# Kernel tuning notes

Hardware: AMD Instinct MI355X
Metric: run time of the kernel (lower is better)

The kernel has to match this reference:

```python
import jax, jax.numpy as jnp
import numpy as np

N = 100000       # n_nodes
E = 128          # hidden_channels
R = 9            # n_relations
L = 3            # n_layers
NE = 640000      # n_edges


def setup_inputs() -> dict:
    key = jax.random.key(0)
    k = jax.random.split(key, 5)
    edge_index = jax.random.randint(k[0], (2, NE), 0, N, dtype=jnp.int64)
    edge_type = jax.random.randint(k[1], (NE,), 0, R, dtype=jnp.int64)
    embeddings = jax.random.normal(k[2], (N, E), dtype=jnp.float32)
    # per-layer weights [L, 2R, E, E] (first R = forward direction, last R = reverse)
    weights = jax.random.normal(k[3], (L, 2 * R, E, E), dtype=jnp.float32)
    biases = jax.random.normal(k[4], (L, 2 * R, E), dtype=jnp.float32)
    return {
        "edge_index": edge_index,
        "edge_type": edge_type,
        "embeddings": embeddings,
        "weights": weights,
        "biases": biases,
    }


def reference(edge_index, edge_type, embeddings, weights, biases):
    src, dst = edge_index[0], edge_index[1]
    n_nodes = embeddings.shape[0]
    n_layers, r2 = weights.shape[0], weights.shape[1]
    n_rel = r2 // 2

    hidden = embeddings
    for l in range(n_layers):
        # NB: source code resets hidden to the embeddings at the top of each
        # layer, so each layer transforms the raw embeddings. We reproduce
        # that exactly (the relu in the source is dead code: its result is
        # immediately overwritten by `hidden = output`).
        hidden = embeddings
        # Transform node features once per relation (node-level GEMM) instead
        # of per-edge: mathematically identical to gathering then matmul.
        ht = jnp.einsum('ne,reh->rnh', hidden, weights[l])  # [2R, N, E]
        # forward direction: message = W_r @ h[src] + b_r, scattered to dst
        msg_f = ht[edge_type, src] + biases[l][edge_type]          # [NE, E]
        out = jax.ops.segment_sum(msg_f, dst, num_segments=n_nodes)
        # reverse direction: message = W_{r+R} @ h[dst] + b_{r+R}, scattered to src
        msg_b = ht[edge_type + n_rel, dst] + biases[l][edge_type + n_rel]
        out = out + jax.ops.segment_sum(msg_b, src, num_segments=n_nodes)
        hidden = out
    return hidden
```

## Files before the change

### kernel.cpp

```cpp
#include <hip/hip_runtime.h>
#include <hip/hip_bf16.h>


#define E_DIM 128
#define R_REL 9
#define TN 16
#define MT_P 1156
#define SCB 1024
#define NSLICE 96

typedef __attribute__((ext_vector_type(8))) short short8v;
typedef __attribute__((ext_vector_type(4))) float f32x4;

static __device__ __forceinline__ unsigned short f2bf(float f) {
    union { float f; unsigned u; } v; v.f = f;
    unsigned u = v.u;
    return (unsigned short)((u + 0x7FFFu + ((u >> 16) & 1u)) >> 16);
}
static __device__ __forceinline__ float bf2f(unsigned short h) {
    union { unsigned u; float f; } v; v.u = ((unsigned)h) << 16;
    return v.f;
}


__global__ __launch_bounds__(256) void prep(
    const float* __restrict__ H, const float* __restrict__ W18,
    unsigned short* __restrict__ Hbf, unsigned short* __restrict__ Wt,
    long total8)
{
    const int tid = threadIdx.x;
    if (blockIdx.x < 18) {
        const int rel = blockIdx.x;
        const float* __restrict__ Wr = W18 + (size_t)rel * E_DIM * E_DIM;
#pragma unroll
        for (int k = 0; k < 8; k++) {
            int f = tid + k * 256;
            int lane = f & 63;
            int c = (f >> 6) & 1;
            int s = (f >> 7) & 3;
            int w = (f >> 9) & 3;
            int col = w * 32 + c * 16 + (lane & 15);
            int kb = s * 32 + (lane >> 4) * 8;
            short8v v;
#pragma unroll
            for (int j = 0; j < 8; j++)
                v[j] = (short)f2bf(Wr[(size_t)(kb + j) * E_DIM + col]);
            *(short8v*)(Wt + ((size_t)((((rel * 4 + w) * 4 + s) * 2 + c) * 64 + lane)) * 8) = v;
        }
    } else {
        long i = (long)(blockIdx.x - 18) * 256 + tid;
        if (i >= total8) return;
        const float4* src = (const float4*)(H + i * 8);
        float4 a = src[0], b = src[1];
        short8v o;
        o[0] = (short)f2bf(a.x); o[1] = (short)f2bf(a.y);
        o[2] = (short)f2bf(a.z); o[3] = (short)f2bf(a.w);
        o[4] = (short)f2bf(b.x); o[5] = (short)f2bf(b.y);
        o[6] = (short)f2bf(b.z); o[7] = (short)f2bf(b.w);
        *(short8v*)(Hbf + i * 8) = o;
    }
}

__global__ __launch_bounds__(256) void k_count8(
    const int* __restrict__ esrc, const int* __restrict__ edst,
    const int* __restrict__ etype, int* __restrict__ cnt, int ne, int Nn)
{
    const int oct = blockIdx.x & 7;
    const int slice = blockIdx.x >> 3;
    const int lo = (int)(((long long)oct * Nn) >> 3);
    const int hi = (int)(((long long)(oct + 1) * Nn) >> 3);
    for (int e = slice * 256 + threadIdx.x; e < ne; e += NSLICE * 256) {
        int t = etype[e], s = esrc[e], d = edst[e];
        if (d >= lo && d < hi) atomicAdd(&cnt[d * R_REL + t], 1);
        if (s >= lo && s < hi) atomicAdd(&cnt[(Nn + s) * R_REL + t], 1);
    }
}

__global__ __launch_bounds__(256) void k_scan_part(
    const int* __restrict__ cnt, int* __restrict__ loc,
    int* __restrict__ bsum, int n2)
{
    __shared__ int sh[256];
    const int tid = threadIdx.x;
    const int i0 = blockIdx.x * SCB + tid * 4;
    int v0 = 0, v1 = 0, v2 = 0, v3 = 0;
    if (i0 + 3 < n2) {
        int4 v = *(const int4*)(cnt + i0);
        v0 = v.x; v1 = v.y; v2 = v.z; v3 = v.w;
    } else {
        if (i0 + 0 < n2) v0 = cnt[i0 + 0];
        if (i0 + 1 < n2) v1 = cnt[i0 + 1];
        if (i0 + 2 < n2) v2 = cnt[i0 + 2];
        if (i0 + 3 < n2) v3 = cnt[i0 + 3];
    }
    int t = v0 + v1 + v2 + v3;
    sh[tid] = t;
    __syncthreads();
    for (int o = 1; o < 256; o <<= 1) {
        int x = (tid >= o) ? sh[tid - o] : 0;
        __syncthreads();
        sh[tid] += x;
        __syncthreads();
    }
    int excl = sh[tid] - t;
    if (tid == 255) bsum[blockIdx.x] = sh[255];
    int p0 = excl, p1 = p0 + v0, p2 = p1 + v1, p3 = p2 + v2;
    if (i0 + 3 < n2) {
        *(int4*)(loc + i0) = make_int4(p0, p1, p2, p3);
    } else {
        if (i0 + 0 < n2) loc[i0 + 0] = p0;
        if (i0 + 1 < n2) loc[i0 + 1] = p1;
        if (i0 + 2 < n2) loc[i0 + 2] = p2;
        if (i0 + 3 < n2) loc[i0 + 3] = p3;
    }
}

__global__ __launch_bounds__(256) void k_scan_mid(int* __restrict__ bsum, int nb)
{
    __shared__ int sh[256];
    __shared__ int carry;
    const int tid = threadIdx.x;
    if (tid == 0) carry = 0;
    __syncthreads();
    for (int base = 0; base < nb; base += 256) {
        int i = base + tid;
        int v = (i < nb) ? bsum[i] : 0;
        sh[tid] = v;
        __syncthreads();
        for (int o = 1; o < 256; o <<= 1) {
            int x = (tid >= o) ? sh[tid - o] : 0;
            __syncthreads();
            sh[tid] += x;
            __syncthreads();
        }
        int excl = sh[tid] - v + carry;
        int total = sh[255];
        if (i < nb) bsum[i] = excl;
        __syncthreads();
        if (tid == 0) carry += total;
        __syncthreads();
    }
}

__global__ __launch_bounds__(256) void k_scan_apply(
    const int* __restrict__ loc, const int* __restrict__ bsum,
    int* __restrict__ off, int* __restrict__ cursor, int n2)
{
    const int add = bsum[blockIdx.x];
    const int i0 = blockIdx.x * SCB + threadIdx.x * 4;
    if (i0 + 3 < n2) {
        int4 v = *(const int4*)(loc + i0);
        v.x += add; v.y += add; v.z += add; v.w += add;
        *(int4*)(off + i0) = v;
        *(int4*)(cursor + i0) = v;
    } else {
#pragma unroll
        for (int j = 0; j < 4; j++)
            if (i0 + j < n2) {
                int v = loc[i0 + j] + add;
                off[i0 + j] = v;
                cursor[i0 + j] = v;
            }
    }
}

__global__ __launch_bounds__(256) void k_fill8(
    const int* __restrict__ esrc, const int* __restrict__ edst,
    const int* __restrict__ etype, int* __restrict__ cursor,
    unsigned* __restrict__ rec, int ne, int Nn)
{
    const int oct = blockIdx.x & 7;
    const int slice = blockIdx.x >> 3;
    const int lo = (int)(((long long)oct * Nn) >> 3);
    const int hi = (int)(((long long)(oct + 1) * Nn) >> 3);
    for (int e = slice * 256 + threadIdx.x; e < ne; e += NSLICE * 256) {
        int t = etype[e], s = esrc[e], d = edst[e];
        if (d >= lo && d < hi) {
            int p = atomicAdd(&cursor[d * R_REL + t], 1);
            rec[p] = ((unsigned)t << 20) | (unsigned)s;
        }
        if (s >= lo && s < hi) {
            int p2 = atomicAdd(&cursor[(Nn + s) * R_REL + t], 1);
            rec[p2] = ((unsigned)t << 20) | (unsigned)d;
        }
    }
}

__global__ __launch_bounds__(256, 4) void fused_rgcn(
    const unsigned short* __restrict__ Hbf, const unsigned short* __restrict__ Wt,
    const float* __restrict__ B18,
    const int* __restrict__ off3, const int* __restrict__ cur3,
    const unsigned* __restrict__ rec,
    float* __restrict__ out, int Nn)
{
    __shared__ __align__(16) unsigned short Mt[TN][MT_P];
    __shared__ float degS[2][TN][R_REL];

    const int tid = threadIdx.x;
    const int lane = tid & 63;
    const int w = tid >> 6;
    const int lr = lane & 15;
    const int lg = lane >> 4;
    const int n0 = blockIdx.x * TN;

    const short8v* wt8 = (const short8v*)Wt;

    f32x4 acc[2];
    acc[0] = (f32x4){0.f, 0.f, 0.f, 0.f};
    acc[1] = (f32x4){0.f, 0.f, 0.f, 0.f};

#define RMW(rk, vk, idx)                                                      \
    {                                                                         \
        int _t = (rk) >> 20;                                                  \
        int _nd = ((idx) >= s1) + ((idx) >= s2) + ((idx) >= s3);              \
        unsigned* _mp = (unsigned*)(&Mt[w * 4 + _nd][_t * E_DIM]) + lane;     \
        unsigned _u = *_mp;                                                   \
        float _mx = bf2f((unsigned short)(_u & 0xFFFF)) + bf2f((vk).x);       \
        float _my = bf2f((unsigned short)(_u >> 16)) + bf2f((vk).y);          \
        *_mp = ((unsigned)f2bf(_my) << 16) | (unsigned)f2bf(_mx);             \
    }

#pragma unroll 1
    for (int dir = 0; dir < 2; dir++) {
        const short8v z8 = (short8v){0, 0, 0, 0, 0, 0, 0, 0};
#pragma unroll
        for (int rr = 0; rr < 4; rr++) {
            int row = w * 4 + rr;
            *(short8v*)(&Mt[row][(size_t)lane * 8]) = z8;
            *(short8v*)(&Mt[row][(size_t)(lane + 64) * 8]) = z8;
            if (lane < 16) *(short8v*)(&Mt[row][(size_t)(lane + 128) * 8]) = z8;
        }

        const int jj = lg, tt = lr;
        const int gnode_j = n0 + w * 4 + jj;
        int blo = 0x7F000000, bhi = 0x7F000000;
        if (gnode_j < Nn && tt < R_REL) {
            size_t sb = ((size_t)(dir ? (Nn + gnode_j) : gnode_j)) * R_REL + tt;
            blo = off3[sb];
            bhi = cur3[sb];
            degS[dir][w * 4 + jj][tt] = (float)(bhi - blo);
        }

        const int nvalid = min(4, max(0, Nn - (n0 + w * 4)));
        const int st = __shfl(blo, 0);
        const int en = (nvalid > 0) ? __shfl(bhi, (nvalid - 1) * 16 + 8) : -1;
        const int s1 = __shfl(blo, 16);
        const int s2 = __shfl(blo, 32);
        const int s3 = __shfl(blo, 48);

        int i = st;
        for (; i + 8 <= en; i += 8) {
            unsigned rv = rec[i + (lane & 7)];
            int r0 = __builtin_amdgcn_readlane(rv, 0);
            int r1 = __builtin_amdgcn_readlane(rv, 1);
            int r2 = __builtin_amdgcn_readlane(rv, 2);
            int r3 = __builtin_amdgcn_readlane(rv, 3);
            int r4 = __builtin_amdgcn_readlane(rv, 4);
            int r5 = __builtin_amdgcn_readlane(rv, 5);
            int r6 = __builtin_amdgcn_readlane(rv, 6);
            int r7 = __builtin_amdgcn_readlane(rv, 7);
            ushort2 v0 = *(const ushort2*)(Hbf + (size_t)(r0 & 0xFFFFF) * E_DIM + 2 * lane);
            ushort2 v1 = *(const ushort2*)(Hbf + (size_t)(r1 & 0xFFFFF) * E_DIM + 2 * lane);
            ushort2 v2 = *(const ushort2*)(Hbf + (size_t)(r2 & 0xFFFFF) * E_DIM + 2 * lane);
            ushort2 v3 = *(const ushort2*)(Hbf + (size_t)(r3 & 0xFFFFF) * E_DIM + 2 * lane);
            ushort2 v4 = *(const ushort2*)(Hbf + (size_t)(r4 & 0xFFFFF) * E_DIM + 2 * lane);
            ushort2 v5 = *(const ushort2*)(Hbf + (size_t)(r5 & 0xFFFFF) * E_DIM + 2 * lane);
            ushort2 v6 = *(const ushort2*)(Hbf + (size_t)(r6 & 0xFFFFF) * E_DIM + 2 * lane);
            ushort2 v7 = *(const ushort2*)(Hbf + (size_t)(r7 & 0xFFFFF) * E_DIM + 2 * lane);
            RMW(r0, v0, i + 0);
            RMW(r1, v1, i + 1);
            RMW(r2, v2, i + 2);
            RMW(r3, v3, i + 3);
            RMW(r4, v4, i + 4);
            RMW(r5, v5, i + 5);
            RMW(r6, v6, i + 6);
            RMW(r7, v7, i + 7);
        }
        for (; i < en; i++) {
            int rk = __builtin_amdgcn_readfirstlane((int)rec[i]);
            ushort2 vk = *(const ushort2*)(Hbf + (size_t)(rk & 0xFFFFF) * E_DIM + 2 * lane);
            RMW(rk, vk, i);
        }
        __syncthreads();

#pragma unroll 1
        for (int q = 0; q < R_REL; q++) {
            const int rel = dir * R_REL + q;
#pragma unroll
            for (int s = 0; s < 4; s++) {
                short8v b0 = wt8[(size_t)((((rel * 4 + w) * 4 + s) * 2 + 0) * 64) + lane];
                short8v b1 = wt8[(size_t)((((rel * 4 + w) * 4 + s) * 2 + 1) * 64) + lane];
                short8v a = *(const short8v*)(&Mt[lr][q * E_DIM + s * 32 + lg * 8]);
                acc[0] = __builtin_amdgcn_mfma_f32_16x16x32_bf16(b0, a, acc[0], 0, 0, 0);
                acc[1] = __builtin_amdgcn_mfma_f32_16x16x32_bf16(b1, a, acc[1], 0, 0, 0);
            }
        }
        __syncthreads();
    }
#undef RMW

    const int gnode = n0 + lr;
    if (gnode >= Nn) return;
#pragma unroll 1
    for (int dir = 0; dir < 2; dir++) {
#pragma unroll 1
        for (int t = 0; t < R_REL; t++) {
            float dg = degS[dir][lr][t];
            if (dg != 0.f) {
                const float* brow = B18 + (size_t)(dir * R_REL + t) * E_DIM + w * 32 + lg * 4;
                float4 b0 = *(const float4*)(brow);
                float4 b1 = *(const float4*)(brow + 16);
                acc[0][0] += dg * b0.x; acc[0][1] += dg * b0.y;
                acc[0][2] += dg * b0.z; acc[0][3] += dg * b0.w;
                acc[1][0] += dg * b1.x; acc[1][1] += dg * b1.y;
                acc[1][2] += dg * b1.z; acc[1][3] += dg * b1.w;
            }
        }
    }
    float* po = out + (size_t)gnode * E_DIM + w * 32 + lg * 4;
    *(float4*)po = make_float4(acc[0][0], acc[0][1], acc[0][2], acc[0][3]);
    *(float4*)(po + 16) = make_float4(acc[1][0], acc[1][1], acc[1][2], acc[1][3]);
}


__global__ __launch_bounds__(128) void direct_edge(
    const int* __restrict__ esrc, const int* __restrict__ edst,
    const int* __restrict__ etype,
    const float* __restrict__ H, const float* __restrict__ W2,
    const float* __restrict__ B2, float* __restrict__ out, int ne)
{
    __shared__ float hs[E_DIM];
    __shared__ float hd[E_DIM];
    int e = blockIdx.x;
    if (e >= ne) return;
    int t = etype[e], s = esrc[e], d = edst[e];
    int c = threadIdx.x;
    hs[c] = H[(size_t)s * E_DIM + c];
    hd[c] = H[(size_t)d * E_DIM + c];
    __syncthreads();
    const float* Wf = W2 + (size_t)t * E_DIM * E_DIM;
    const float* Wb = W2 + (size_t)(t + R_REL) * E_DIM * E_DIM;
    float accf = B2[(size_t)t * E_DIM + c];
    float accb = B2[(size_t)(t + R_REL) * E_DIM + c];
#pragma unroll 8
    for (int k = 0; k < E_DIM; k++) {
        accf += hs[k] * Wf[(size_t)k * E_DIM + c];
        accb += hd[k] * Wb[(size_t)k * E_DIM + c];
    }
    atomicAdd(&out[(size_t)d * E_DIM + c], accf);
    atomicAdd(&out[(size_t)s * E_DIM + c], accb);
}

extern "C" void kernel_launch(void* const* d_in, const int* in_sizes, int n_in,
                              void* d_out, int out_size, void* d_ws, size_t ws_size,
                              hipStream_t stream) {
    const int* edge_index = (const int*)d_in[0];
    const int* edge_type  = (const int*)d_in[1];
    const float* emb      = (const float*)d_in[2];
    const float* weights  = (const float*)d_in[3];
    const float* biases   = (const float*)d_in[4];
    float* out = (float*)d_out;

    const int NE = in_sizes[1];
    const int Nn = in_sizes[2] / E_DIM;
    const int L  = in_sizes[3] / (2 * R_REL * E_DIM * E_DIM);

    const float* W2 = weights + (size_t)(L - 1) * 2 * R_REL * E_DIM * E_DIM;
    const float* B2 = biases  + (size_t)(L - 1) * 2 * R_REL * E_DIM;

    const int* esrc = edge_index;
    const int* edst = edge_index + NE;

    const int n3 = 2 * Nn * R_REL;
    const int nb3 = (n3 + SCB - 1) / SCB;

    auto al = [](size_t x) { return (x + 255) & ~(size_t)255; };
    const size_t hbfBytes = al((size_t)Nn * E_DIM * 2);
    const size_t wtBytes  = al((size_t)2 * R_REL * E_DIM * E_DIM * 2);
    const size_t offBytes = al((size_t)n3 * 4);
    const size_t curBytes = al((size_t)n3 * 4);
    const size_t recBytes = al((size_t)2 * NE * 4);
    const size_t bsBytes  = al((size_t)nb3 * 4);
    const size_t need = hbfBytes + wtBytes + offBytes + curBytes + recBytes + bsBytes;

    if (ws_size >= need && Nn < (1 << 20)) {
        char* p = (char*)d_ws;
        unsigned short* Hbf = (unsigned short*)p;        p += hbfBytes;
        unsigned short* Wt  = (unsigned short*)p;        p += wtBytes;
        int* off3           = (int*)p;                   p += offBytes;
        int* cur3           = (int*)p;                   p += curBytes;
        unsigned* rec       = (unsigned*)p;              p += recBytes;
        int* bsum           = (int*)p;

        const long total8 = (long)Nn * (E_DIM / 8);
        const int hblocks = (int)((total8 + 255) / 256);

        hipMemsetAsync(off3, 0, (size_t)n3 * 4, stream);
        prep<<<18 + hblocks, 256, 0, stream>>>(emb, W2, Hbf, Wt, total8);
        k_count8<<<8 * NSLICE, 256, 0, stream>>>(esrc, edst, edge_type, off3, NE, Nn);
        k_scan_part<<<nb3, 256, 0, stream>>>(off3, cur3, bsum, n3);
        k_scan_mid<<<1, 256, 0, stream>>>(bsum, nb3);
        k_scan_apply<<<nb3, 256, 0, stream>>>(cur3, bsum, off3, cur3, n3);
        k_fill8<<<8 * NSLICE, 256, 0, stream>>>(esrc, edst, edge_type,
                                                cur3, rec, NE, Nn);

        fused_rgcn<<<(Nn + TN - 1) / TN, 256, 0, stream>>>(
            Hbf, Wt, B2, off3, cur3, rec, out, Nn);
        return;
    }

    hipMemsetAsync(d_out, 0, (size_t)Nn * E_DIM * sizeof(float), stream);
    direct_edge<<<NE, 128, 0, stream>>>(esrc, edst, edge_type, emb, W2, B2, out, NE);
}
```

Before: 414.4 us.

## Process four destination nodes per wave in parallel with 16-byte gathers

Each wave now splits into four 16-lane groups, and each group walks the edge list of its own node instead of the whole wave walking all four nodes' edges serially. Each lane loads 8 bf16 values (16 bytes) per edge row rather than 2, and accumulates into its own shared-memory slot, so the per-edge node-index computation goes away. The aim is more independent gathers in flight and fewer loop iterations per wave. In exchange, groups with uneven edge counts leave lanes idle, the loop unroll drops from 8 to 4, and the record reads are now per-lane loads instead of scalar broadcasts.

```diff
diff --git a/kernel.cpp b/kernel.cpp
--- a/kernel.cpp
+++ b/kernel.cpp
@@ -201,28 +201,33 @@
     const int w = tid >> 6;
     const int lr = lane & 15;
     const int lg = lane >> 4;
+    const int grp = lg;
+    const int gl = lr;
     const int n0 = blockIdx.x * TN;
 
     const short8v* wt8 = (const short8v*)Wt;
+    const short8v z8 = (short8v){0, 0, 0, 0, 0, 0, 0, 0};
 
     f32x4 acc[2];
     acc[0] = (f32x4){0.f, 0.f, 0.f, 0.f};
     acc[1] = (f32x4){0.f, 0.f, 0.f, 0.f};
 
-#define RMW(rk, vk, idx)                                                      \
+#define RMW(rk, vk)                                                           \
     {                                                                         \
-        int _t = (rk) >> 20;                                                  \
-        int _nd = ((idx) >= s1) + ((idx) >= s2) + ((idx) >= s3);              \
-        unsigned* _mp = (unsigned*)(&Mt[w * 4 + _nd][_t * E_DIM]) + lane;     \
-        unsigned _u = *_mp;                                                   \
-        float _mx = bf2f((unsigned short)(_u & 0xFFFF)) + bf2f((vk).x);       \
-        float _my = bf2f((unsigned short)(_u >> 16)) + bf2f((vk).y);          \
-        *_mp = ((unsigned)f2bf(_my) << 16) | (unsigned)f2bf(_mx);             \
+        int _t = (int)((rk) >> 20);                                           \
+        unsigned short* _mp = &Mt[w * 4 + grp][_t * E_DIM + gl * 8];          \
+        short8v _m = *(short8v*)_mp;                                          \
+        _Pragma("unroll")                                                     \
+        for (int _c = 0; _c < 8; _c++) {                                      \
+            float _f = bf2f((unsigned short)_m[_c]) +                         \
+                       bf2f((unsigned short)(vk)[_c]);                        \
+            _m[_c] = (short)f2bf(_f);                                         \
+        }                                                                     \
+        *(short8v*)_mp = _m;                                                  \
     }
 
 #pragma unroll 1
     for (int dir = 0; dir < 2; dir++) {
-        const short8v z8 = (short8v){0, 0, 0, 0, 0, 0, 0, 0};
 #pragma unroll
         for (int rr = 0; rr < 4; rr++) {
             int row = w * 4 + rr;
@@ -241,45 +246,30 @@
             degS[dir][w * 4 + jj][tt] = (float)(bhi - blo);
         }
 
-        const int nvalid = min(4, max(0, Nn - (n0 + w * 4)));
-        const int st = __shfl(blo, 0);
-        const int en = (nvalid > 0) ? __shfl(bhi, (nvalid - 1) * 16 + 8) : -1;
-        const int s1 = __shfl(blo, 16);
-        const int s2 = __shfl(blo, 32);
-        const int s3 = __shfl(blo, 48);
-
-        int i = st;
-        for (; i + 8 <= en; i += 8) {
-            unsigned rv = rec[i + (lane & 7)];
-            int r0 = __builtin_amdgcn_readlane(rv, 0);
-            int r1 = __builtin_amdgcn_readlane(rv, 1);
-            int r2 = __builtin_amdgcn_readlane(rv, 2);
-            int r3 = __builtin_amdgcn_readlane(rv, 3);
-            int r4 = __builtin_amdgcn_readlane(rv, 4);
-            int r5 = __builtin_amdgcn_readlane(rv, 5);
-            int r6 = __builtin_amdgcn_readlane(rv, 6);
-            int r7 = __builtin_amdgcn_readlane(rv, 7);
-            ushort2 v0 = *(const ushort2*)(Hbf + (size_t)(r0 & 0xFFFFF) * E_DIM + 2 * lane);
-            ushort2 v1 = *(const ushort2*)(Hbf + (size_t)(r1 & 0xFFFFF) * E_DIM + 2 * lane);
-            ushort2 v2 = *(const ushort2*)(Hbf + (size_t)(r2 & 0xFFFFF) * E_DIM + 2 * lane);
-            ushort2 v3 = *(const ushort2*)(Hbf + (size_t)(r3 & 0xFFFFF) * E_DIM + 2 * lane);
-            ushort2 v4 = *(const ushort2*)(Hbf + (size_t)(r4 & 0xFFFFF) * E_DIM + 2 * lane);
-            ushort2 v5 = *(const ushort2*)(Hbf + (size_t)(r5 & 0xFFFFF) * E_DIM + 2 * lane);
-            ushort2 v6 = *(const ushort2*)(Hbf + (size_t)(r6 & 0xFFFFF) * E_DIM + 2 * lane);
-            ushort2 v7 = *(const ushort2*)(Hbf + (size_t)(r7 & 0xFFFFF) * E_DIM + 2 * lane);
-            RMW(r0, v0, i + 0);
-            RMW(r1, v1, i + 1);
-            RMW(r2, v2, i + 2);
-            RMW(r3, v3, i + 3);
-            RMW(r4, v4, i + 4);
-            RMW(r5, v5, i + 5);
-            RMW(r6, v6, i + 6);
-            RMW(r7, v7, i + 7);
-        }
-        for (; i < en; i++) {
-            int rk = __builtin_amdgcn_readfirstlane((int)rec[i]);
-            ushort2 vk = *(const ushort2*)(Hbf + (size_t)(rk & 0xFFFFF) * E_DIM + 2 * lane);
-            RMW(rk, vk, i);
+        const int st_g = __shfl(blo, grp * 16 + 0);
+        const int en_g = __shfl(bhi, grp * 16 + 8);
+
+        int ii = st_g;
+        while (__any(ii < en_g)) {
+            bool a0 = ii + 0 < en_g;
+            bool a1 = ii + 1 < en_g;
+            bool a2 = ii + 2 < en_g;
+            bool a3 = ii + 3 < en_g;
+            unsigned r0 = 0, r1 = 0, r2 = 0, r3 = 0;
+            if (a0) r0 = rec[ii + 0];
+            if (a1) r1 = rec[ii + 1];
+            if (a2) r2 = rec[ii + 2];
+            if (a3) r3 = rec[ii + 3];
+            short8v v0 = z8, v1 = z8, v2 = z8, v3 = z8;
+            if (a0) v0 = *(const short8v*)(Hbf + (size_t)(r0 & 0xFFFFF) * E_DIM + gl * 8);
+            if (a1) v1 = *(const short8v*)(Hbf + (size_t)(r1 & 0xFFFFF) * E_DIM + gl * 8);
+            if (a2) v2 = *(const short8v*)(Hbf + (size_t)(r2 & 0xFFFFF) * E_DIM + gl * 8);
+            if (a3) v3 = *(const short8v*)(Hbf + (size_t)(r3 & 0xFFFFF) * E_DIM + gl * 8);
+            if (a0) RMW(r0, v0);
+            if (a1) RMW(r1, v1);
+            if (a2) RMW(r2, v2);
+            if (a3) RMW(r3, v3);
+            ii += 4;
         }
         __syncthreads();
 
```

Result: no change. 414.6 us (+0.1%).
